# Optimization experiments

Measured on AMD Instinct MI355X. Metric: run time of the kernel, lower is better.

The kernel has to match this reference:

```python
import math
import jax, jax.numpy as jnp
import numpy as np

ALPHA = 12.0  # agg_alpha
TAU = 0.07


def setup_inputs() -> dict:
    key = jax.random.key(0)
    kq, kk, kqm, kkm = jax.random.split(key, 4)
    B, Lq, O, Lk, D = 64, 32, 128, 256, 128
    q = jax.random.normal(kq, (B, Lq, D), dtype=jnp.float32)
    k = jax.random.normal(kk, (O, Lk, D), dtype=jnp.float32)
    # True = padding token (masked out)
    q_mask = jax.random.bernoulli(kqm, 0.1, (B, Lq))
    k_mask = jax.random.bernoulli(kkm, 0.1, (O, Lk))
    logit_scale = jnp.asarray(math.log(1.0 / TAU), dtype=jnp.float32)
    return {"q": q, "k": k, "q_mask": q_mask, "k_mask": k_mask,
            "logit_scale": logit_scale}


def _l2norm(x, eps=1e-12):
    # torch F.normalize: x / max(||x||_2, eps)
    n = jnp.sqrt(jnp.sum(x * x, axis=-1, keepdims=True))
    return x / jnp.maximum(n, eps)


def reference(q, k, q_mask, k_mask, logit_scale):
    B, Lq, D = q.shape
    O, Lk, _ = k.shape
    qn = _l2norm(q)
    kn = _l2norm(k)
    # S: [B, O, Lq, Lk] full similarity tensor (the kernel-headroom intermediate)
    S = jnp.einsum('bid,ojd->boij', qn, kn)
    m = q_mask[:, None, :, None] | k_mask[None, :, None, :]
    S = jnp.where(m, -jnp.inf, S)
    # softmax-pool over Lk: logsumexp(alpha*S)/alpha, then sum over Lq
    s = jax.nn.logsumexp(ALPHA * S, axis=-1) / ALPHA  # [B, O, Lq]
    s = jnp.sum(s, axis=-1)                            # [B, O]
    s = jnp.where(jnp.isfinite(s), s, jnp.zeros_like(s))
    # length_norm = 'sqrt'
    s = s / (math.sqrt(Lq * Lk) + 1e-06)
    # learnable temperature, exp clamped at 100
    scale = jnp.minimum(jnp.exp(logit_scale), 100.0)
    return s * scale
```

## Files before the change

### kernel.cpp

```cpp
#include <hip/hip_runtime.h>
#include <math.h>


#define ALPHA 12.0f

constexpr int B_  = 64;
constexpr int LQ  = 32;
constexpr int O_  = 128;
constexpr int LK  = 256;
constexpr int D_  = 128;
constexpr int LDH = D_ + 8;

typedef _Float16 half8   __attribute__((ext_vector_type(8)));
typedef _Float16 half4_t __attribute__((ext_vector_type(4)));
typedef float    f32x4   __attribute__((ext_vector_type(4)));

__global__ __launch_bounds__(256, 1)
void colbert_fused_kernel(const float* __restrict__ q,
                          const float* __restrict__ k,
                          const int*  __restrict__ q_mask,
                          const int*  __restrict__ k_mask,
                          const float* __restrict__ logit_scale,
                          float* __restrict__ out)
{
    __shared__ _Float16 kl[LK][LDH];
    __shared__ _Float16 ql[LQ][LDH];
    __shared__ float rk[LK];
    __shared__ float bj[LK];
    __shared__ float rqa[LQ];
    __shared__ float part[2][LQ];
    __shared__ int   deadf[B_];
    __shared__ int   lbm[B_ + 1];

    const int o     = blockIdx.x;
    const int t     = threadIdx.x;
    const int lane  = t & 63;
    const int w     = t >> 6;
    const int row16 = lane & 15;
    const int quad  = lane >> 4;

    {
        const int4* qm4 = (const int4*)q_mask;
        int4 a0 = qm4[t * 2], a1 = qm4[t * 2 + 1];
        int any = a0.x | a0.y | a0.z | a0.w | a1.x | a1.y | a1.z | a1.w;
        any |= __shfl_xor(any, 1);
        any |= __shfl_xor(any, 2);
        if ((t & 3) == 0) {
            int b = t >> 2;
            deadf[b] = any;
            if (any) out[b * O_ + o] = 0.0f;
        }
    }
    __syncthreads();
    if (t < 64) {
        bool live = (deadf[t] == 0);
        unsigned long long m = __ballot(live);
        if (live) {
            int rank = __popcll(m & ((1ull << t) - 1ull));
            lbm[1 + rank] = t;
        }
        if (t == 0) lbm[0] = (int)__popcll(m);
    }
    __syncthreads();
    const int M = lbm[0];
    if (M == 0) return;

    {
        const float4* kg = (const float4*)(k + (size_t)o * LK * D_);
        #pragma unroll 8
        for (int r = 0; r < 32; ++r) {
            int idx = t + 256 * r;
            float4 v = kg[idx];
            int j = idx >> 5, c4 = idx & 31;
            half4_t h;
            h[0] = (_Float16)v.x; h[1] = (_Float16)v.y;
            h[2] = (_Float16)v.z; h[3] = (_Float16)v.w;
            *(half4_t*)&kl[j][c4 * 4] = h;
        }
    }
    __syncthreads();
    {
        float ss = 0.f;
        #pragma unroll
        for (int p = 0; p < 16; ++p) {
            half8 h = *(const half8*)&kl[t][p * 8];
            #pragma unroll
            for (int e = 0; e < 8; ++e) {
                float x = (float)h[e];
                ss = fmaf(x, x, ss);
            }
        }
        rk[t] = 1.0f / fmaxf(sqrtf(ss), 1e-12f);
        bj[t] = (k_mask[o * LK + t] != 0) ? -1e30f : 0.0f;
    }

    const float scale  = fminf(__expf(logit_scale[0]), 100.0f);
    const float inv_ln = 1.0f / (sqrtf((float)(LQ * LK)) + 1e-6f);

    for (int m = 0; m < M; ++m) {
        const int b = lbm[1 + m];

        const float4* qg = (const float4*)(q + (size_t)b * LQ * D_);
        #pragma unroll
        for (int r = 0; r < 4; ++r) {
            int idx = t + 256 * r;
            float4 v = qg[idx];
            int i = idx >> 5, c4 = idx & 31;
            half4_t h;
            h[0] = (_Float16)v.x; h[1] = (_Float16)v.y;
            h[2] = (_Float16)v.z; h[3] = (_Float16)v.w;
            *(half4_t*)&ql[i][c4 * 4] = h;
        }
        __syncthreads();

        if (t < LQ) {
            float ss = 0.f;
            #pragma unroll
            for (int p = 0; p < 16; ++p) {
                half8 h = *(const half8*)&ql[t][p * 8];
                #pragma unroll
                for (int e = 0; e < 8; ++e) {
                    float x = (float)h[e];
                    ss = fmaf(x, x, ss);
                }
            }
            rqa[t] = ALPHA / fmaxf(sqrtf(ss), 1e-12f);
        }
        __syncthreads();

        const int i0 = (w >> 1) * 16;
        const int j0 = (w & 1) * 128;

        half8 afrag[4];
        #pragma unroll
        for (int kk = 0; kk < 4; ++kk)
            afrag[kk] = *(const half8*)&ql[i0 + row16][kk * 32 + quad * 8];

        float rqv[4];
        #pragma unroll
        for (int rg = 0; rg < 4; ++rg)
            rqv[rg] = rqa[i0 + quad * 4 + rg];

        float esum[4] = {0.f, 0.f, 0.f, 0.f};
        #pragma unroll
        for (int c = 0; c < 8; ++c) {
            const int jt = j0 + c * 16;
            f32x4 acc = {0.f, 0.f, 0.f, 0.f};
            #pragma unroll
            for (int kk = 0; kk < 4; ++kk) {
                half8 bfrag = *(const half8*)&kl[jt + row16][kk * 32 + quad * 8];
                acc = __builtin_amdgcn_mfma_f32_16x16x32_f16(afrag[kk], bfrag,
                                                             acc, 0, 0, 0);
            }
            const float rkj = rk[jt + row16];
            const float bb  = bj[jt + row16];
            #pragma unroll
            for (int rg = 0; rg < 4; ++rg)
                esum[rg] += __expf(acc[rg] * rqv[rg] * rkj + bb);
        }
        #pragma unroll
        for (int rg = 0; rg < 4; ++rg) {
            float e = esum[rg];
            e += __shfl_xor(e, 1);
            e += __shfl_xor(e, 2);
            e += __shfl_xor(e, 4);
            e += __shfl_xor(e, 8);
            esum[rg] = e;
        }
        if (row16 == 0) {
            #pragma unroll
            for (int rg = 0; rg < 4; ++rg)
                part[w & 1][i0 + quad * 4 + rg] = esum[rg];
        }
        __syncthreads();

        if (t < 64) {
            float s = 0.f, lse = 0.f;
            bool badrow = false;
            if (t < LQ) {
                s = part[0][t] + part[1][t];
                badrow = (s <= 0.f);
                lse = __logf(fmaxf(s, 1e-38f));
            }
            unsigned long long zb = __ballot(badrow);
            float tot = lse;
            tot += __shfl_xor(tot, 32);
            tot += __shfl_xor(tot, 16);
            tot += __shfl_xor(tot, 8);
            tot += __shfl_xor(tot, 4);
            tot += __shfl_xor(tot, 2);
            tot += __shfl_xor(tot, 1);
            if (t == 0) {
                float res = 0.f;
                if (zb == 0ULL)
                    res = (tot * (1.0f / ALPHA)) * inv_ln * scale;
                out[b * O_ + o] = res;
            }
        }
    }
}

extern "C" void kernel_launch(void* const* d_in, const int* in_sizes, int n_in,
                              void* d_out, int out_size, void* d_ws, size_t ws_size,
                              hipStream_t stream) {
    const float* q           = (const float*)d_in[0];
    const float* k           = (const float*)d_in[1];
    const int*   q_mask      = (const int*)d_in[2];
    const int*   k_mask      = (const int*)d_in[3];
    const float* logit_scale = (const float*)d_in[4];
    float* out = (float*)d_out;

    colbert_fused_kernel<<<O_, 256, 0, stream>>>(q, k, q_mask, k_mask,
                                                 logit_scale, out);
}
```

Measured before the change: 76.11 us.

## Process two live queries per iteration and prefetch K before mask scan

Each block now handles two live batch queries per loop iteration. Both share each K fragment loaded from LDS across two MFMAs, and the per-query barriers and reductions are paid once per pair. The K tile is loaded into registers in two 16-float4 batches, issued together with the q_mask loads so global latency overlaps the mask check. The live-batch list in shared memory is replaced by a ballot mask walked with ctz. This raises register pressure from the larger K staging arrays and doubled accumulators, and with an odd number of live queries the last query is computed twice.

```diff
diff --git a/kernel.cpp b/kernel.cpp
--- a/kernel.cpp
+++ b/kernel.cpp
@@ -24,13 +24,11 @@
                           float* __restrict__ out)
 {
     __shared__ _Float16 kl[LK][LDH];
-    __shared__ _Float16 ql[LQ][LDH];
+    __shared__ _Float16 ql2[2][LQ][LDH];
     __shared__ float rk[LK];
-    __shared__ float bj[LK];
-    __shared__ float rqa[LQ];
-    __shared__ float part[2][LQ];
-    __shared__ int   deadf[B_];
-    __shared__ int   lbm[B_ + 1];
+    __shared__ float bjs[LK];
+    __shared__ float rqa2[2][LQ];
+    __shared__ float part2[2][2][LQ];
 
     const int o     = blockIdx.x;
     const int t     = threadIdx.x;
@@ -39,162 +37,191 @@
     const int row16 = lane & 15;
     const int quad  = lane >> 4;
 
+    int4 mm[8];
     {
         const int4* qm4 = (const int4*)q_mask;
-        int4 a0 = qm4[t * 2], a1 = qm4[t * 2 + 1];
-        int any = a0.x | a0.y | a0.z | a0.w | a1.x | a1.y | a1.z | a1.w;
-        any |= __shfl_xor(any, 1);
-        any |= __shfl_xor(any, 2);
-        if ((t & 3) == 0) {
-            int b = t >> 2;
-            deadf[b] = any;
-            if (any) out[b * O_ + o] = 0.0f;
-        }
+        #pragma unroll
+        for (int u = 0; u < 8; ++u)
+            mm[u] = qm4[lane * 8 + u];
+    }
+
+    const float4* kg = (const float4*)(k + (size_t)o * LK * D_);
+    float4 kv[16];
+    #pragma unroll
+    for (int r = 0; r < 16; ++r)
+        kv[r] = kg[t + 256 * r];
+    const int   km = k_mask[o * LK + t];
+    const float ls = logit_scale[0];
+
+    int any = 0;
+    #pragma unroll
+    for (int u = 0; u < 8; ++u)
+        any |= mm[u].x | mm[u].y | mm[u].z | mm[u].w;
+    const bool live = (any == 0);
+    const unsigned long long mball = __ballot(live);
+    if (w == 0 && !live) out[lane * O_ + o] = 0.0f;
+    const int M = (int)__popcll(mball);
+    if (M == 0) return;
+
+    #pragma unroll
+    for (int r = 0; r < 16; ++r) {
+        int idx = t + 256 * r;
+        int j = idx >> 5, c4 = idx & 31;
+        half4_t hh;
+        hh[0] = (_Float16)kv[r].x; hh[1] = (_Float16)kv[r].y;
+        hh[2] = (_Float16)kv[r].z; hh[3] = (_Float16)kv[r].w;
+        *(half4_t*)&kl[j][c4 * 4] = hh;
+    }
+    #pragma unroll
+    for (int r = 0; r < 16; ++r)
+        kv[r] = kg[4096 + t + 256 * r];
+    #pragma unroll
+    for (int r = 0; r < 16; ++r) {
+        int idx = 4096 + t + 256 * r;
+        int j = idx >> 5, c4 = idx & 31;
+        half4_t hh;
+        hh[0] = (_Float16)kv[r].x; hh[1] = (_Float16)kv[r].y;
+        hh[2] = (_Float16)kv[r].z; hh[3] = (_Float16)kv[r].w;
+        *(half4_t*)&kl[j][c4 * 4] = hh;
     }
     __syncthreads();
-    if (t < 64) {
-        bool live = (deadf[t] == 0);
-        unsigned long long m = __ballot(live);
-        if (live) {
-            int rank = __popcll(m & ((1ull << t) - 1ull));
-            lbm[1 + rank] = t;
-        }
-        if (t == 0) lbm[0] = (int)__popcll(m);
-    }
-    __syncthreads();
-    const int M = lbm[0];
-    if (M == 0) return;
-
-    {
-        const float4* kg = (const float4*)(k + (size_t)o * LK * D_);
-        #pragma unroll 8
-        for (int r = 0; r < 32; ++r) {
-            int idx = t + 256 * r;
-            float4 v = kg[idx];
-            int j = idx >> 5, c4 = idx & 31;
-            half4_t h;
-            h[0] = (_Float16)v.x; h[1] = (_Float16)v.y;
-            h[2] = (_Float16)v.z; h[3] = (_Float16)v.w;
-            *(half4_t*)&kl[j][c4 * 4] = h;
-        }
-    }
-    __syncthreads();
+
     {
         float ss = 0.f;
         #pragma unroll
         for (int p = 0; p < 16; ++p) {
-            half8 h = *(const half8*)&kl[t][p * 8];
+            half8 hh = *(const half8*)&kl[t][p * 8];
             #pragma unroll
             for (int e = 0; e < 8; ++e) {
-                float x = (float)h[e];
+                float x = (float)hh[e];
                 ss = fmaf(x, x, ss);
             }
         }
-        rk[t] = 1.0f / fmaxf(sqrtf(ss), 1e-12f);
-        bj[t] = (k_mask[o * LK + t] != 0) ? -1e30f : 0.0f;
-    }
-
-    const float scale  = fminf(__expf(logit_scale[0]), 100.0f);
+        rk[t]  = 1.0f / fmaxf(sqrtf(ss), 1e-12f);
+        bjs[t] = (km != 0) ? -1e30f : 0.0f;
+    }
+
+    const float scale  = fminf(__expf(ls), 100.0f);
     const float inv_ln = 1.0f / (sqrtf((float)(LQ * LK)) + 1e-6f);
 
-    for (int m = 0; m < M; ++m) {
-        const int b = lbm[1 + m];
-
-        const float4* qg = (const float4*)(q + (size_t)b * LQ * D_);
+    unsigned long long mrem = mball;
+    for (int m0 = 0; m0 < M; m0 += 2) {
+        const int b0 = (int)__builtin_ctzll(mrem); mrem &= mrem - 1ull;
+        int b1 = b0;
+        if (m0 + 1 < M) { b1 = (int)__builtin_ctzll(mrem); mrem &= mrem - 1ull; }
+
+        const float4* qg0 = (const float4*)(q + (size_t)b0 * LQ * D_);
+        const float4* qg1 = (const float4*)(q + (size_t)b1 * LQ * D_);
         #pragma unroll
         for (int r = 0; r < 4; ++r) {
             int idx = t + 256 * r;
-            float4 v = qg[idx];
+            float4 v0 = qg0[idx];
+            float4 v1 = qg1[idx];
             int i = idx >> 5, c4 = idx & 31;
-            half4_t h;
-            h[0] = (_Float16)v.x; h[1] = (_Float16)v.y;
-            h[2] = (_Float16)v.z; h[3] = (_Float16)v.w;
-            *(half4_t*)&ql[i][c4 * 4] = h;
+            half4_t h0, h1;
+            h0[0] = (_Float16)v0.x; h0[1] = (_Float16)v0.y;
+            h0[2] = (_Float16)v0.z; h0[3] = (_Float16)v0.w;
+            h1[0] = (_Float16)v1.x; h1[1] = (_Float16)v1.y;
+            h1[2] = (_Float16)v1.z; h1[3] = (_Float16)v1.w;
+            *(half4_t*)&ql2[0][i][c4 * 4] = h0;
+            *(half4_t*)&ql2[1][i][c4 * 4] = h1;
         }
         __syncthreads();
 
-        if (t < LQ) {
+        if (t < 64) {
+            const int pb = t >> 5, i = t & 31;
             float ss = 0.f;
             #pragma unroll
             for (int p = 0; p < 16; ++p) {
-                half8 h = *(const half8*)&ql[t][p * 8];
+                half8 hh = *(const half8*)&ql2[pb][i][p * 8];
                 #pragma unroll
                 for (int e = 0; e < 8; ++e) {
-                    float x = (float)h[e];
+                    float x = (float)hh[e];
                     ss = fmaf(x, x, ss);
                 }
             }
-            rqa[t] = ALPHA / fmaxf(sqrtf(ss), 1e-12f);
+            rqa2[pb][i] = ALPHA / fmaxf(sqrtf(ss), 1e-12f);
         }
         __syncthreads();
 
         const int i0 = (w >> 1) * 16;
         const int j0 = (w & 1) * 128;
 
-        half8 afrag[4];
-        #pragma unroll
-        for (int kk = 0; kk < 4; ++kk)
-            afrag[kk] = *(const half8*)&ql[i0 + row16][kk * 32 + quad * 8];
-
-        float rqv[4];
-        #pragma unroll
-        for (int rg = 0; rg < 4; ++rg)
-            rqv[rg] = rqa[i0 + quad * 4 + rg];
-
-        float esum[4] = {0.f, 0.f, 0.f, 0.f};
+        half8 afrag[2][4];
+        #pragma unroll
+        for (int pb = 0; pb < 2; ++pb)
+            #pragma unroll
+            for (int kk = 0; kk < 4; ++kk)
+                afrag[pb][kk] =
+                    *(const half8*)&ql2[pb][i0 + row16][kk * 32 + quad * 8];
+
+        float rqv[2][4];
+        #pragma unroll
+        for (int pb = 0; pb < 2; ++pb)
+            #pragma unroll
+            for (int rg = 0; rg < 4; ++rg)
+                rqv[pb][rg] = rqa2[pb][i0 + quad * 4 + rg];
+
+        float esum[2][4] = {{0.f,0.f,0.f,0.f},{0.f,0.f,0.f,0.f}};
         #pragma unroll
         for (int c = 0; c < 8; ++c) {
             const int jt = j0 + c * 16;
-            f32x4 acc = {0.f, 0.f, 0.f, 0.f};
+            f32x4 acc0 = {0.f, 0.f, 0.f, 0.f};
+            f32x4 acc1 = {0.f, 0.f, 0.f, 0.f};
             #pragma unroll
             for (int kk = 0; kk < 4; ++kk) {
-                half8 bfrag = *(const half8*)&kl[jt + row16][kk * 32 + quad * 8];
-                acc = __builtin_amdgcn_mfma_f32_16x16x32_f16(afrag[kk], bfrag,
-                                                             acc, 0, 0, 0);
+                half8 bfrag =
+                    *(const half8*)&kl[jt + row16][kk * 32 + quad * 8];
+                acc0 = __builtin_amdgcn_mfma_f32_16x16x32_f16(
+                           afrag[0][kk], bfrag, acc0, 0, 0, 0);
+                acc1 = __builtin_amdgcn_mfma_f32_16x16x32_f16(
+                           afrag[1][kk], bfrag, acc1, 0, 0, 0);
             }
             const float rkj = rk[jt + row16];
-            const float bb  = bj[jt + row16];
-            #pragma unroll
-            for (int rg = 0; rg < 4; ++rg)
-                esum[rg] += __expf(acc[rg] * rqv[rg] * rkj + bb);
-        }
-        #pragma unroll
-        for (int rg = 0; rg < 4; ++rg) {
-            float e = esum[rg];
-            e += __shfl_xor(e, 1);
-            e += __shfl_xor(e, 2);
-            e += __shfl_xor(e, 4);
-            e += __shfl_xor(e, 8);
-            esum[rg] = e;
-        }
-        if (row16 == 0) {
-            #pragma unroll
-            for (int rg = 0; rg < 4; ++rg)
-                part[w & 1][i0 + quad * 4 + rg] = esum[rg];
+            const float bb  = bjs[jt + row16];
+            #pragma unroll
+            for (int rg = 0; rg < 4; ++rg) {
+                esum[0][rg] += __expf(acc0[rg] * rqv[0][rg] * rkj + bb);
+                esum[1][rg] += __expf(acc1[rg] * rqv[1][rg] * rkj + bb);
+            }
+        }
+        #pragma unroll
+        for (int pb = 0; pb < 2; ++pb) {
+            #pragma unroll
+            for (int rg = 0; rg < 4; ++rg) {
+                float e = esum[pb][rg];
+                e += __shfl_xor(e, 1);
+                e += __shfl_xor(e, 2);
+                e += __shfl_xor(e, 4);
+                e += __shfl_xor(e, 8);
+                esum[pb][rg] = e;
+            }
+            if (row16 == 0)
+                #pragma unroll
+                for (int rg = 0; rg < 4; ++rg)
+                    part2[pb][w & 1][i0 + quad * 4 + rg] = esum[pb][rg];
         }
         __syncthreads();
 
         if (t < 64) {
-            float s = 0.f, lse = 0.f;
-            bool badrow = false;
-            if (t < LQ) {
-                s = part[0][t] + part[1][t];
-                badrow = (s <= 0.f);
-                lse = __logf(fmaxf(s, 1e-38f));
-            }
-            unsigned long long zb = __ballot(badrow);
+            const int pb = t >> 5, i = t & 31;
+            float s = part2[pb][0][i] + part2[pb][1][i];
+            bool badrow = (s <= 0.f);
+            float lse = __logf(fmaxf(s, 1e-38f));
             float tot = lse;
-            tot += __shfl_xor(tot, 32);
             tot += __shfl_xor(tot, 16);
             tot += __shfl_xor(tot, 8);
             tot += __shfl_xor(tot, 4);
             tot += __shfl_xor(tot, 2);
             tot += __shfl_xor(tot, 1);
-            if (t == 0) {
+            unsigned long long zb = __ballot(badrow);
+            if (i == 0) {
+                unsigned long long half_mask =
+                    (pb == 0) ? 0xFFFFFFFFull : 0xFFFFFFFF00000000ull;
                 float res = 0.f;
-                if (zb == 0ULL)
+                if ((zb & half_mask) == 0ull)
                     res = (tot * (1.0f / ALPHA)) * inv_ln * scale;
-                out[b * O_ + o] = res;
+                out[((pb == 0) ? b0 : b1) * O_ + o] = res;
             }
         }
     }
```

Result: no change. 76.97 us (+1.1%).
